# Optimization experiments

Measured on AMD Instinct MI355X. Metric: run time of the kernel, lower is better.

The kernel has to match this reference:

```python
import jax, jax.numpy as jnp
import numpy as np

EPS = 1e-7
B, C, H, W = 8, 128, 256, 256
HEADS, P = 8, 8
P2 = P * P  # 64
KSIZE = 3


def setup_inputs() -> dict:
    key = jax.random.key(0)
    ks = jax.random.split(key, 9)
    s = 0.05
    x = jax.random.normal(ks[0], (B, C, H, W), jnp.float32)
    Wq = jax.random.normal(ks[1], (P2 * HEADS, P2), jnp.float32) * s
    bq = jax.random.normal(ks[2], (P2 * HEADS,), jnp.float32) * s
    Wk = jax.random.normal(ks[3], (P2 * HEADS, P2), jnp.float32) * s
    bk = jax.random.normal(ks[4], (P2 * HEADS,), jnp.float32) * s
    Wv = jax.random.normal(ks[5], (C, C), jnp.float32) * s  # 1x1 conv squeezed
    bv = jax.random.normal(ks[6], (C,), jnp.float32) * s
    Wp = jax.random.normal(ks[7], (C, 1, KSIZE, KSIZE), jnp.float32) * s  # depthwise
    bp = jax.random.normal(ks[8], (C,), jnp.float32) * s
    return {"x": x, "Wq": Wq, "bq": bq, "Wk": Wk, "bk": bk,
            "Wv": Wv, "bv": bv, "Wp": Wp, "bp": bp}


def _linear_attn(q, k, xv):
    # q, k: [B, heads, C, P2]; xv: [B, heads, C, d2]
    l1, d1 = q.shape[-2], q.shape[-1]
    l2, d2 = xv.shape[-2], xv.shape[-1]
    if l1 * d1 * l2 + l1 * l2 * d2 <= d2 * l2 * d1 + d2 * d1 * l1:
        qk = jnp.einsum('bhcp,bhdp->bhcd', q, k)          # q @ k^T : [B,h,C,C]
        qk = qk / (qk.sum(axis=-1, keepdims=True) + EPS)
        return jnp.einsum('bhcd,bhde->bhce', qk, xv)
    else:
        kx = jnp.einsum('bhcp,bhcd->bhpd', k, xv)          # k^T @ x : [B,h,P2,d2]
        out = jnp.einsum('bhcp,bhpd->bhcd', q, kx)         # q @ (k^T @ x)
        denom = jnp.einsum('bhcp,bhp->bhc', q, k.sum(axis=2)) + EPS  # q @ rowsum(k^T)
        return out / denom[..., None]


def reference(x, Wq, bq, Wk, bk, Wv, bv, Wp, bp):
    Bs, Cs, Hs, Ws = x.shape
    # AdaptiveAvgPool2d(P) with divisible dims == block mean
    pooled = x.reshape(Bs, Cs, P, Hs // P, P, Ws // P).mean(axis=(3, 5))
    pooled = pooled.reshape(Bs, Cs, P2)
    q = jax.nn.relu(pooled @ Wq.T + bq).reshape(Bs, Cs, HEADS, P2).transpose(0, 2, 1, 3)
    k = jax.nn.relu(pooled @ Wk.T + bk).reshape(Bs, Cs, HEADS, P2).transpose(0, 2, 1, 3)
    # 1x1 conv (v)
    v = jnp.einsum('bchw,oc->bohw', x, Wv) + bv[None, :, None, None]
    d2 = (Hs * Ws) // HEADS  # divisible by construction -> no replicate pad
    xv = v.reshape(Bs, Cs, HEADS, d2).transpose(0, 2, 1, 3)
    attn = _linear_attn(q, k, xv)                           # [B,h,C,d2]
    out = attn.transpose(0, 2, 1, 3).reshape(Bs, Cs, Hs, Ws)
    # depthwise 3x3 proj, padding 1
    out = jax.lax.conv_general_dilated(
        out, Wp, window_strides=(1, 1), padding=[(1, 1), (1, 1)],
        dimension_numbers=('NCHW', 'OIHW', 'NCHW'), feature_group_count=Cs)
    return out + bp[None, :, None, None]
```

## Files before the change

### kernel.cpp

```cpp
#include <hip/hip_runtime.h>
#include <hip/hip_bf16.h>

#define HW 65536
#define CCH 128

typedef __attribute__((ext_vector_type(8))) short short8;
typedef __attribute__((ext_vector_type(4))) float f32x4;
typedef __attribute__((ext_vector_type(8))) unsigned short u16x8;

__device__ __forceinline__ void gload_lds16(const void* g, void* l) {
    __builtin_amdgcn_global_load_lds((const __attribute__((address_space(1))) void*)g,
                                     (__attribute__((address_space(3))) void*)l, 16, 0, 0);
}
__device__ __forceinline__ unsigned short f2bf(float f) {
    union { float f; unsigned int i; } u; u.f = f;
    unsigned int r = u.i + 0x7fffu + ((u.i >> 16) & 1u);
    return (unsigned short)(r >> 16);
}
__device__ __forceinline__ float bf2f(unsigned short h) {
    union { unsigned int i; float f; } u; u.i = ((unsigned int)h) << 16; return u.f;
}

__global__ __launch_bounds__(256) void pool_kernel(const float* __restrict__ x,
                                                   float* __restrict__ pooled) {
    int bc = blockIdx.x;
    const float* base = x + (size_t)bc * HW;
    int t = threadIdx.x;
    for (int py = 0; py < 8; ++py) {
        float acc = 0.f;
        const float* rowp = base + py * 32 * 256 + t;
        #pragma unroll
        for (int r = 0; r < 32; ++r) acc += rowp[r * 256];
        for (int off = 16; off > 0; off >>= 1) acc += __shfl_down(acc, off, 32);
        if ((t & 31) == 0)
            pooled[(size_t)bc * 64 + py * 8 + (t >> 5)] = acc * (1.0f / 1024.0f);
    }
}

__global__ __launch_bounds__(256) void qk_kernel(const float* __restrict__ pooled,
        const float* __restrict__ Wq, const float* __restrict__ bq,
        const float* __restrict__ Wk, const float* __restrict__ bk,
        float* __restrict__ qo, float* __restrict__ ko) {
    int bc = blockIdx.x;
    int t = threadIdx.x;
    __shared__ float ps[64];
    if (t < 64) ps[t] = pooled[(size_t)bc * 64 + t];
    __syncthreads();
    for (int m = 0; m < 2; ++m) {
        const float* W = m ? Wk : Wq;
        const float* bb = m ? bk : bq;
        float* o = m ? ko : qo;
        for (int oi = t; oi < 512; oi += 256) {
            float acc = bb[oi];
            const float* wr = W + oi * 64;
            #pragma unroll
            for (int p = 0; p < 64; ++p) acc += ps[p] * wr[p];
            o[(size_t)bc * 512 + oi] = fmaxf(acc, 0.f);
        }
    }
}

__global__ __launch_bounds__(256) void am1_kernel(const float* __restrict__ q,
        const float* __restrict__ k, const float* __restrict__ bv,
        unsigned short* __restrict__ Ahi, unsigned short* __restrict__ Alo,
        float* __restrict__ beta) {
    int bid = blockIdx.x;
    int bh = bid >> 2;
    int cg = bid & 3;
    int b = bh >> 3, h = bh & 7;
    int t = threadIdx.x;
    __shared__ float ks[128 * 68];
    __shared__ float qs[32 * 68];
    __shared__ float bvs[128];
    for (int i = t; i < 2048; i += 256) {
        int d = i >> 4, p4 = (i & 15) * 4;
        *(f32x4*)&ks[d * 68 + p4] = *(const f32x4*)(k + ((size_t)(b * CCH + d)) * 512 + h * 64 + p4);
    }
    for (int i = t; i < 512; i += 256) {
        int cl = i >> 4, p4 = (i & 15) * 4;
        *(f32x4*)&qs[cl * 68 + p4] = *(const f32x4*)(q + ((size_t)(b * CCH + cg * 32 + cl)) * 512 + h * 64 + p4);
    }
    if (t < 128) bvs[t] = bv[t];
    __syncthreads();
    int cl = t >> 3, dc = t & 7;
    int c = cg * 32 + cl;
    int d0 = dc * 16;
    f32x4 qr[16];
    #pragma unroll
    for (int ch = 0; ch < 16; ++ch) qr[ch] = *(const f32x4*)&qs[cl * 68 + ch * 4];
    float a[16];
    #pragma unroll
    for (int j = 0; j < 16; ++j) {
        int d = d0 + j;
        float acc = 0.f;
        #pragma unroll
        for (int ch = 0; ch < 16; ++ch) {
            f32x4 kr = *(const f32x4*)&ks[d * 68 + ch * 4];
            acc += qr[ch].x * kr.x + qr[ch].y * kr.y + qr[ch].z * kr.z + qr[ch].w * kr.w;
        }
        a[j] = acc;
    }
    float s = 0.f;
    #pragma unroll
    for (int j = 0; j < 16; ++j) s += a[j];
    s += __shfl_xor(s, 1);
    s += __shfl_xor(s, 2);
    s += __shfl_xor(s, 4);
    float inv = 1.0f / (s + 1e-7f);
    float bpart = 0.f;
    union { unsigned short u[16]; uint4 v[2]; } ph, pl;
    #pragma unroll
    for (int j = 0; j < 16; ++j) {
        float an = a[j] * inv;
        bpart += an * bvs[d0 + j];
        unsigned short hi = f2bf(an);
        ph.u[j] = hi;
        pl.u[j] = f2bf(an - bf2f(hi));
    }
    bpart += __shfl_xor(bpart, 1);
    bpart += __shfl_xor(bpart, 2);
    bpart += __shfl_xor(bpart, 4);
    if (dc == 0) beta[bh * 128 + c] = bpart;
    size_t ao = (size_t)bh * 16384 + c * 128 + d0;
    *(uint4*)(Ahi + ao) = ph.v[0];
    *(uint4*)(Ahi + ao + 8) = ph.v[1];
    *(uint4*)(Alo + ao) = pl.v[0];
    *(uint4*)(Alo + ao + 8) = pl.v[1];
}

__global__ __launch_bounds__(256) void wvt_kernel(const float* __restrict__ Wv,
        unsigned short* __restrict__ WvThi, unsigned short* __restrict__ WvTlo) {
    int idx = blockIdx.x * 256 + threadIdx.x;
    int d = idx >> 7, e = idx & 127;
    float v = Wv[d * 128 + e];
    unsigned short hi = f2bf(v);
    WvThi[e * 128 + d] = hi;
    WvTlo[e * 128 + d] = f2bf(v - bf2f(hi));
}

__global__ __launch_bounds__(256) void am2_kernel(
        const unsigned short* __restrict__ Ahi, const unsigned short* __restrict__ Alo,
        const unsigned short* __restrict__ WvThi, const unsigned short* __restrict__ WvTlo,
        unsigned short* __restrict__ Mo) {
    int bid = blockIdx.x;
    int bh = bid >> 1;
    int eg = bid & 1;
    int tid = threadIdx.x;
    int w = tid >> 6, l = tid & 63;
    int lc = l & 15, lk = (l >> 4) * 8;
    f32x4 acc[2][4] = {};
    const unsigned short* Ab = Ahi + (size_t)bh * 16384;
    const unsigned short* Alb = Alo + (size_t)bh * 16384;
    #pragma unroll
    for (int ksi = 0; ksi < 4; ++ksi) {
        int d = ksi * 32 + lk;
        short8 ah[2], al[2], bhv[4], blv[4];
        #pragma unroll
        for (int ci = 0; ci < 2; ++ci) {
            int c = w * 32 + ci * 16 + lc;
            ah[ci] = *(const short8*)(Ab + c * 128 + d);
            al[ci] = *(const short8*)(Alb + c * 128 + d);
        }
        #pragma unroll
        for (int ei = 0; ei < 4; ++ei) {
            int e = eg * 64 + ei * 16 + lc;
            bhv[ei] = *(const short8*)(WvThi + e * 128 + d);
            blv[ei] = *(const short8*)(WvTlo + e * 128 + d);
        }
        #pragma unroll
        for (int ci = 0; ci < 2; ++ci)
            #pragma unroll
            for (int ei = 0; ei < 4; ++ei) {
                acc[ci][ei] = __builtin_amdgcn_mfma_f32_16x16x32_bf16(ah[ci], bhv[ei], acc[ci][ei], 0, 0, 0);
                acc[ci][ei] = __builtin_amdgcn_mfma_f32_16x16x32_bf16(ah[ci], blv[ei], acc[ci][ei], 0, 0, 0);
                acc[ci][ei] = __builtin_amdgcn_mfma_f32_16x16x32_bf16(al[ci], bhv[ei], acc[ci][ei], 0, 0, 0);
            }
    }
    unsigned short* Mb = Mo + (size_t)bh * 16384;
    #pragma unroll
    for (int ci = 0; ci < 2; ++ci)
        #pragma unroll
        for (int ei = 0; ei < 4; ++ei)
            #pragma unroll
            for (int r = 0; r < 4; ++r) {
                int c = w * 32 + ci * 16 + (l >> 4) * 4 + r;
                int e = eg * 64 + ei * 16 + lc;
                Mb[c * 128 + e] = f2bf(acc[ci][ei][r]);
            }
}

__global__ __launch_bounds__(512, 4) void attn_kernel(
        const float* __restrict__ x,
        const __hip_bfloat16* __restrict__ Mbf,
        const float* __restrict__ beta,
        __hip_bfloat16* __restrict__ attn) {
    int bid = blockIdx.x;
    int bh = bid >> 4;
    int chunk = bid & 15;
    int b = bh >> 3, h = bh & 7;
    int s0g = h * 8192 + chunk * 512;
    int tid = threadIdx.x;
    int w = tid >> 6, l = tid & 63;

    __shared__ __align__(16) char sm[65536];
    char* ts0 = sm + 32768;

    const char* Mg = (const char*)(Mbf + (size_t)bh * 16384);
    #pragma unroll
    for (int i = 0; i < 4; ++i) {
        int o = i * 8192 + tid * 16;
        int osw = o ^ (((o >> 8) & 7) << 4);
        gload_lds16(Mg + osw, sm + o);
    }

    int e0u = (tid >> 4) * 2;
    int s4u = (tid & 15) * 4;
    const float* xb = x + (size_t)b * CCH * HW + s0g;

    f32x4 rg[4];
    #define LOADT(t_) do { \
        const float* p0 = xb + (size_t)e0u * HW + (t_) * 64 + s4u; \
        rg[0] = *(const f32x4*)p0; \
        rg[1] = *(const f32x4*)(p0 + HW); \
        const float* p1 = p0 + (size_t)64 * HW; \
        rg[2] = *(const f32x4*)p1; \
        rg[3] = *(const f32x4*)(p1 + HW); \
    } while (0)
    #define WRITET(buf_) do { \
        _Pragma("unroll") \
        for (int j = 0; j < 4; ++j) { \
            int s = s4u + j; \
            int sw = (s & 7) << 4; \
            unsigned int pa = (unsigned int)f2bf(rg[0][j]) | ((unsigned int)f2bf(rg[1][j]) << 16); \
            unsigned int pb = (unsigned int)f2bf(rg[2][j]) | ((unsigned int)f2bf(rg[3][j]) << 16); \
            *(unsigned int*)((buf_) + ((s * 256 + e0u * 2) ^ sw)) = pa; \
            *(unsigned int*)((buf_) + ((s * 256 + (e0u + 64) * 2) ^ sw)) = pb; \
        } \
    } while (0)

    LOADT(0);
    WRITET(ts0);
    LOADT(1);
    __syncthreads();

    int c0w = (w >> 1) * 32;
    int s0w = (w & 1) * 32;
    short8 mf[2][4];
    #pragma unroll
    for (int ci = 0; ci < 2; ++ci)
        #pragma unroll
        for (int ksi = 0; ksi < 4; ++ksi) {
            int c = c0w + ci * 16 + (l & 15);
            int o = (c * 256 + ksi * 64 + ((l >> 4) * 16)) ^ ((c & 7) << 4);
            mf[ci][ksi] = *(const short8*)(sm + o);
        }
    const float* bet = beta + bh * 128;
    float bv0 = bet[c0w + (l & 15)];
    float bv1 = bet[c0w + 16 + (l & 15)];
    __hip_bfloat16* ab = attn + (size_t)b * CCH * HW + s0g;

    for (int t = 0; t < 8; ++t) {
        char* tsc = ts0 + (t & 1) * 16384;
        if (t < 7) WRITET(ts0 + ((t + 1) & 1) * 16384);
        if (t < 6) LOADT(t + 2);
        f32x4 acc[2][2] = {};
        #pragma unroll
        for (int ksi = 0; ksi < 4; ++ksi) {
            short8 af[2];
            #pragma unroll
            for (int si = 0; si < 2; ++si) {
                int s = s0w + si * 16 + (l & 15);
                int o = (s * 256 + ksi * 64 + ((l >> 4) * 16)) ^ ((s & 7) << 4);
                af[si] = *(const short8*)(tsc + o);
            }
            #pragma unroll
            for (int si = 0; si < 2; ++si)
                #pragma unroll
                for (int ci = 0; ci < 2; ++ci)
                    acc[si][ci] = __builtin_amdgcn_mfma_f32_16x16x32_bf16(af[si], mf[ci][ksi], acc[si][ci], 0, 0, 0);
        }
        #pragma unroll
        for (int si = 0; si < 2; ++si)
            #pragma unroll
            for (int ci = 0; ci < 2; ++ci) {
                int sb = s0w + si * 16 + (l >> 4) * 4;
                int c = c0w + ci * 16 + (l & 15);
                float bvv = ci ? bv1 : bv0;
                union { unsigned short u[4]; uint2 v; } pk;
                #pragma unroll
                for (int r = 0; r < 4; ++r) pk.u[r] = f2bf(acc[si][ci][r] + bvv);
                *(uint2*)(ab + (size_t)c * HW + t * 64 + sb) = pk.v;
            }
        __syncthreads();
    }
    #undef LOADT
    #undef WRITET
}

__global__ __launch_bounds__(256) void dwconv_kernel(const __hip_bfloat16* __restrict__ attn,
        const float* __restrict__ Wp, const float* __restrict__ bp,
        float* __restrict__ out) {
    int bid = blockIdx.x;
    int bc = bid >> 3;
    int ys = bid & 7;
    int y0 = ys * 32;
    int t = threadIdx.x;
    __shared__ unsigned short tile[34][264];
    const unsigned short* base = (const unsigned short*)attn + (size_t)bc * HW;
    for (int i = t; i < 34 * 32; i += 256) {
        int r = i >> 5, ck = i & 31;
        int gy = y0 + r - 1;
        u16x8 v;
        if (gy >= 0 && gy < 256) v = *(const u16x8*)(base + gy * 256 + ck * 8);
        else v = (u16x8)((unsigned short)0);
        *(u16x8*)&tile[r][ck * 8] = v;
    }
    __syncthreads();
    int c = bc & 127;
    float wv[9];
    #pragma unroll
    for (int j = 0; j < 9; ++j) wv[j] = Wp[c * 9 + j];
    float bias = bp[c];
    float* obase = out + (size_t)bc * HW;
    for (int p = 0; p < 4; ++p) {
        int orow = p * 8 + (t >> 5);
        int oc = (t & 31) * 8;
        float accv[8];
        #pragma unroll
        for (int j = 0; j < 8; ++j) accv[j] = bias;
        #pragma unroll
        for (int dy = 0; dy < 3; ++dy) {
            int tr = orow + dy;
            u16x8 m = *(const u16x8*)&tile[tr][oc];
            float f[10];
            f[0] = (oc == 0) ? 0.f : bf2f(tile[tr][oc - 1]);
            #pragma unroll
            for (int j = 0; j < 8; ++j) f[j + 1] = bf2f(m[j]);
            f[9] = (oc == 248) ? 0.f : bf2f(tile[tr][oc + 8]);
            float w0 = wv[dy * 3], w1 = wv[dy * 3 + 1], w2 = wv[dy * 3 + 2];
            #pragma unroll
            for (int j = 0; j < 8; ++j)
                accv[j] += w0 * f[j] + w1 * f[j + 1] + w2 * f[j + 2];
        }
        float* op = obase + (size_t)(y0 + orow) * 256 + oc;
        float4 o0 = {accv[0], accv[1], accv[2], accv[3]};
        float4 o1 = {accv[4], accv[5], accv[6], accv[7]};
        *(float4*)op = o0;
        *(float4*)(op + 4) = o1;
    }
}

extern "C" void kernel_launch(void* const* d_in, const int* in_sizes, int n_in,
                              void* d_out, int out_size, void* d_ws, size_t ws_size,
                              hipStream_t stream) {
    const float* x  = (const float*)d_in[0];
    const float* Wq = (const float*)d_in[1];
    const float* bq = (const float*)d_in[2];
    const float* Wk = (const float*)d_in[3];
    const float* bk = (const float*)d_in[4];
    const float* Wv = (const float*)d_in[5];
    const float* bv = (const float*)d_in[6];
    const float* Wp = (const float*)d_in[7];
    const float* bp = (const float*)d_in[8];
    float* out = (float*)d_out;
    char* ws = (char*)d_ws;

    float* pooled = (float*)ws;
    float* qb     = (float*)(ws + 262144);
    float* kb     = (float*)(ws + 2359296);
    __hip_bfloat16* Mbf = (__hip_bfloat16*)(ws + 4456448);
    float* betab  = (float*)(ws + 6553600);
    char* attnp   = ws + 6586368;
    unsigned short* Ahi   = (unsigned short*)attnp;
    unsigned short* Alo   = (unsigned short*)(attnp + 2097152);
    unsigned short* WvThi = (unsigned short*)(attnp + 4194304);
    unsigned short* WvTlo = (unsigned short*)(attnp + 4227072);

    pool_kernel<<<dim3(1024), dim3(256), 0, stream>>>(x, pooled);
    qk_kernel<<<dim3(1024), dim3(256), 0, stream>>>(pooled, Wq, bq, Wk, bk, qb, kb);
    am1_kernel<<<dim3(256), dim3(256), 0, stream>>>(qb, kb, bv, Ahi, Alo, betab);
    wvt_kernel<<<dim3(64), dim3(256), 0, stream>>>(Wv, WvThi, WvTlo);
    am2_kernel<<<dim3(128), dim3(256), 0, stream>>>(Ahi, Alo, WvThi, WvTlo, (unsigned short*)Mbf);
    attn_kernel<<<dim3(1024), dim3(512), 0, stream>>>(x, Mbf, betab, (__hip_bfloat16*)attnp);
    dwconv_kernel<<<dim3(8192), dim3(256), 0, stream>>>((const __hip_bfloat16*)attnp, Wp, bp, out);
}
```

Measured before the change: 306.5 us.

## Fuse q/k projection into attention-matrix kernel, inline Wv transpose, vectorize pooling

Merges the q/k projection and the attention-matrix construction into one kernel, so q and k are computed straight into LDS and never written to or read back from global memory. The separate Wv transpose/split kernel is removed: each am2 block now builds a swizzled bf16 hi/lo copy of Wv in LDS itself. Pooling switches to f32x4 vector loads with a narrower shuffle reduction, and bf16 packing uses the hardware packed-convert instruction. Together these cut two kernel launches and some global traffic. In exchange, the k projection is recomputed per channel-group block (four times per batch-head), the fused kernel needs a large LDS footprint that may limit occupancy, and the packed convert's rounding may differ slightly from the manual round-to-nearest-even helper.

```diff
diff --git a/kernel.cpp b/kernel.cpp
--- a/kernel.cpp
+++ b/kernel.cpp
@@ -19,6 +19,11 @@
 }
 __device__ __forceinline__ float bf2f(unsigned short h) {
     union { unsigned int i; float f; } u; u.i = ((unsigned int)h) << 16; return u.f;
+}
+__device__ __forceinline__ unsigned int cvt_pk_bf16(float lo, float hi) {
+    unsigned int r;
+    asm("v_cvt_pk_bf16_f32 %0, %1, %2" : "=v"(r) : "v"(lo), "v"(hi));
+    return r;
 }
 
 __global__ __launch_bounds__(256) void pool_kernel(const float* __restrict__ x,
@@ -26,42 +31,32 @@
     int bc = blockIdx.x;
     const float* base = x + (size_t)bc * HW;
     int t = threadIdx.x;
-    for (int py = 0; py < 8; ++py) {
-        float acc = 0.f;
-        const float* rowp = base + py * 32 * 256 + t;
-        #pragma unroll
-        for (int r = 0; r < 32; ++r) acc += rowp[r * 256];
-        for (int off = 16; off > 0; off >>= 1) acc += __shfl_down(acc, off, 32);
-        if ((t & 31) == 0)
-            pooled[(size_t)bc * 64 + py * 8 + (t >> 5)] = acc * (1.0f / 1024.0f);
-    }
-}
-
-__global__ __launch_bounds__(256) void qk_kernel(const float* __restrict__ pooled,
+    int w = t >> 6, l = t & 63;
+    for (int it = 0; it < 2; ++it) {
+        int py = w + it * 4;
+        const float* rp = base + py * 32 * 256 + l * 4;
+        f32x4 s0 = {0.f, 0.f, 0.f, 0.f};
+        f32x4 s1 = {0.f, 0.f, 0.f, 0.f};
+        #pragma unroll
+        for (int r = 0; r < 32; r += 2) {
+            s0 += *(const f32x4*)(rp + r * 256);
+            s1 += *(const f32x4*)(rp + (r + 1) * 256);
+        }
+        f32x4 sv = s0 + s1;
+        float acc = sv[0] + sv[1] + sv[2] + sv[3];
+        acc += __shfl_down(acc, 4, 8);
+        acc += __shfl_down(acc, 2, 8);
+        acc += __shfl_down(acc, 1, 8);
+        if ((l & 7) == 0)
+            pooled[(size_t)bc * 64 + py * 8 + (l >> 3)] = acc * (1.0f / 1024.0f);
+    }
+}
+
+__global__ __launch_bounds__(256) void qkam_kernel(
+        const float* __restrict__ pooled,
         const float* __restrict__ Wq, const float* __restrict__ bq,
         const float* __restrict__ Wk, const float* __restrict__ bk,
-        float* __restrict__ qo, float* __restrict__ ko) {
-    int bc = blockIdx.x;
-    int t = threadIdx.x;
-    __shared__ float ps[64];
-    if (t < 64) ps[t] = pooled[(size_t)bc * 64 + t];
-    __syncthreads();
-    for (int m = 0; m < 2; ++m) {
-        const float* W = m ? Wk : Wq;
-        const float* bb = m ? bk : bq;
-        float* o = m ? ko : qo;
-        for (int oi = t; oi < 512; oi += 256) {
-            float acc = bb[oi];
-            const float* wr = W + oi * 64;
-            #pragma unroll
-            for (int p = 0; p < 64; ++p) acc += ps[p] * wr[p];
-            o[(size_t)bc * 512 + oi] = fmaxf(acc, 0.f);
-        }
-    }
-}
-
-__global__ __launch_bounds__(256) void am1_kernel(const float* __restrict__ q,
-        const float* __restrict__ k, const float* __restrict__ bv,
+        const float* __restrict__ bv,
         unsigned short* __restrict__ Ahi, unsigned short* __restrict__ Alo,
         float* __restrict__ beta) {
     int bid = blockIdx.x;
@@ -69,83 +64,129 @@
     int cg = bid & 3;
     int b = bh >> 3, h = bh & 7;
     int t = threadIdx.x;
+    __shared__ float ps[128 * 64];
+    __shared__ float Wqs[64 * 64];
+    __shared__ float Wks[64 * 64];
     __shared__ float ks[128 * 68];
     __shared__ float qs[32 * 68];
     __shared__ float bvs[128];
+
     for (int i = t; i < 2048; i += 256) {
-        int d = i >> 4, p4 = (i & 15) * 4;
-        *(f32x4*)&ks[d * 68 + p4] = *(const f32x4*)(k + ((size_t)(b * CCH + d)) * 512 + h * 64 + p4);
-    }
-    for (int i = t; i < 512; i += 256) {
-        int cl = i >> 4, p4 = (i & 15) * 4;
-        *(f32x4*)&qs[cl * 68 + p4] = *(const f32x4*)(q + ((size_t)(b * CCH + cg * 32 + cl)) * 512 + h * 64 + p4);
+        int c = i >> 4, p4 = (i & 15) * 4;
+        *(f32x4*)&ps[c * 64 + p4] = *(const f32x4*)(pooled + (size_t)(b * CCH + c) * 64 + p4);
+    }
+    for (int i = t; i < 1024; i += 256) {
+        int r = i >> 4, p4 = (i & 15) * 4;
+        *(f32x4*)&Wqs[r * 64 + p4] = *(const f32x4*)(Wq + (size_t)(h * 64 + r) * 64 + p4);
+        *(f32x4*)&Wks[r * 64 + p4] = *(const f32x4*)(Wk + (size_t)(h * 64 + r) * 64 + p4);
     }
     if (t < 128) bvs[t] = bv[t];
     __syncthreads();
-    int cl = t >> 3, dc = t & 7;
-    int c = cg * 32 + cl;
-    int d0 = dc * 16;
-    f32x4 qr[16];
-    #pragma unroll
-    for (int ch = 0; ch < 16; ++ch) qr[ch] = *(const f32x4*)&qs[cl * 68 + ch * 4];
-    float a[16];
-    #pragma unroll
-    for (int j = 0; j < 16; ++j) {
-        int d = d0 + j;
-        float acc = 0.f;
-        #pragma unroll
-        for (int ch = 0; ch < 16; ++ch) {
-            f32x4 kr = *(const f32x4*)&ks[d * 68 + ch * 4];
-            acc += qr[ch].x * kr.x + qr[ch].y * kr.y + qr[ch].z * kr.z + qr[ch].w * kr.w;
-        }
-        a[j] = acc;
-    }
-    float s = 0.f;
-    #pragma unroll
-    for (int j = 0; j < 16; ++j) s += a[j];
-    s += __shfl_xor(s, 1);
-    s += __shfl_xor(s, 2);
-    s += __shfl_xor(s, 4);
-    float inv = 1.0f / (s + 1e-7f);
-    float bpart = 0.f;
-    union { unsigned short u[16]; uint4 v[2]; } ph, pl;
-    #pragma unroll
-    for (int j = 0; j < 16; ++j) {
-        float an = a[j] * inv;
-        bpart += an * bvs[d0 + j];
-        unsigned short hi = f2bf(an);
-        ph.u[j] = hi;
-        pl.u[j] = f2bf(an - bf2f(hi));
-    }
-    bpart += __shfl_xor(bpart, 1);
-    bpart += __shfl_xor(bpart, 2);
-    bpart += __shfl_xor(bpart, 4);
-    if (dc == 0) beta[bh * 128 + c] = bpart;
-    size_t ao = (size_t)bh * 16384 + c * 128 + d0;
-    *(uint4*)(Ahi + ao) = ph.v[0];
-    *(uint4*)(Ahi + ao + 8) = ph.v[1];
-    *(uint4*)(Alo + ao) = pl.v[0];
-    *(uint4*)(Alo + ao + 8) = pl.v[1];
-}
-
-__global__ __launch_bounds__(256) void wvt_kernel(const float* __restrict__ Wv,
-        unsigned short* __restrict__ WvThi, unsigned short* __restrict__ WvTlo) {
-    int idx = blockIdx.x * 256 + threadIdx.x;
-    int d = idx >> 7, e = idx & 127;
-    float v = Wv[d * 128 + e];
-    unsigned short hi = f2bf(v);
-    WvThi[e * 128 + d] = hi;
-    WvTlo[e * 128 + d] = f2bf(v - bf2f(hi));
+
+    {
+        int p = t & 63, g = t >> 6;
+        f32x4 wr[16];
+        #pragma unroll
+        for (int j = 0; j < 16; ++j) wr[j] = *(const f32x4*)&Wks[p * 64 + j * 4];
+        float bkv = bk[h * 64 + p];
+        for (int dd = 0; dd < 32; ++dd) {
+            int d = g * 32 + dd;
+            float acc = bkv;
+            #pragma unroll
+            for (int j = 0; j < 16; ++j) {
+                f32x4 pv = *(const f32x4*)&ps[d * 64 + j * 4];
+                acc += pv[0] * wr[j][0] + pv[1] * wr[j][1] + pv[2] * wr[j][2] + pv[3] * wr[j][3];
+            }
+            ks[d * 68 + p] = fmaxf(acc, 0.f);
+        }
+        #pragma unroll
+        for (int j = 0; j < 16; ++j) wr[j] = *(const f32x4*)&Wqs[p * 64 + j * 4];
+        float bqv = bq[h * 64 + p];
+        for (int dd = 0; dd < 8; ++dd) {
+            int cl = g * 8 + dd;
+            int c = cg * 32 + cl;
+            float acc = bqv;
+            #pragma unroll
+            for (int j = 0; j < 16; ++j) {
+                f32x4 pv = *(const f32x4*)&ps[c * 64 + j * 4];
+                acc += pv[0] * wr[j][0] + pv[1] * wr[j][1] + pv[2] * wr[j][2] + pv[3] * wr[j][3];
+            }
+            qs[cl * 68 + p] = fmaxf(acc, 0.f);
+        }
+    }
+    __syncthreads();
+
+    {
+        int cl = t >> 3, dc = t & 7;
+        int c = cg * 32 + cl;
+        int d0 = dc * 16;
+        f32x4 qr[16];
+        #pragma unroll
+        for (int ch = 0; ch < 16; ++ch) qr[ch] = *(const f32x4*)&qs[cl * 68 + ch * 4];
+        float a[16];
+        #pragma unroll
+        for (int jr = 0; jr < 16; ++jr) {
+            int j = (jr + dc * 2) & 15;
+            int d = d0 + j;
+            float acc = 0.f;
+            #pragma unroll
+            for (int ch = 0; ch < 16; ++ch) {
+                f32x4 kr = *(const f32x4*)&ks[d * 68 + ch * 4];
+                acc += qr[ch][0] * kr[0] + qr[ch][1] * kr[1] + qr[ch][2] * kr[2] + qr[ch][3] * kr[3];
+            }
+            a[j] = acc;
+        }
+        float s = 0.f;
+        #pragma unroll
+        for (int j = 0; j < 16; ++j) s += a[j];
+        s += __shfl_xor(s, 1);
+        s += __shfl_xor(s, 2);
+        s += __shfl_xor(s, 4);
+        float inv = 1.0f / (s + 1e-7f);
+        float bpart = 0.f;
+        union { unsigned short u[16]; uint4 v[2]; } ph, pl;
+        #pragma unroll
+        for (int j = 0; j < 16; ++j) {
+            float an = a[j] * inv;
+            bpart += an * bvs[d0 + j];
+            unsigned short hi = f2bf(an);
+            ph.u[j] = hi;
+            pl.u[j] = f2bf(an - bf2f(hi));
+        }
+        bpart += __shfl_xor(bpart, 1);
+        bpart += __shfl_xor(bpart, 2);
+        bpart += __shfl_xor(bpart, 4);
+        if (dc == 0) beta[bh * 128 + c] = bpart;
+        size_t ao = (size_t)bh * 16384 + c * 128 + d0;
+        *(uint4*)(Ahi + ao) = ph.v[0];
+        *(uint4*)(Ahi + ao + 8) = ph.v[1];
+        *(uint4*)(Alo + ao) = pl.v[0];
+        *(uint4*)(Alo + ao + 8) = pl.v[1];
+    }
 }
 
 __global__ __launch_bounds__(256) void am2_kernel(
         const unsigned short* __restrict__ Ahi, const unsigned short* __restrict__ Alo,
-        const unsigned short* __restrict__ WvThi, const unsigned short* __restrict__ WvTlo,
-        unsigned short* __restrict__ Mo) {
+        const float* __restrict__ Wv, unsigned short* __restrict__ Mo) {
     int bid = blockIdx.x;
     int bh = bid >> 1;
     int eg = bid & 1;
     int tid = threadIdx.x;
+    __shared__ __align__(16) char Wt[65536];
+    for (int i = tid; i < 4096; i += 256) {
+        int d = i >> 5, e4 = (i & 31) * 4;
+        f32x4 v = *(const f32x4*)(Wv + (size_t)d * 128 + e4);
+        #pragma unroll
+        for (int j = 0; j < 4; ++j) {
+            int e = e4 + j;
+            unsigned short hi = f2bf(v[j]);
+            unsigned short lo = f2bf(v[j] - bf2f(hi));
+            int o = (e * 256 + d * 2) ^ ((e & 7) << 4);
+            *(unsigned short*)(Wt + o) = hi;
+            *(unsigned short*)(Wt + 32768 + o) = lo;
+        }
+    }
+    __syncthreads();
     int w = tid >> 6, l = tid & 63;
     int lc = l & 15, lk = (l >> 4) * 8;
     f32x4 acc[2][4] = {};
@@ -164,8 +205,9 @@
         #pragma unroll
         for (int ei = 0; ei < 4; ++ei) {
             int e = eg * 64 + ei * 16 + lc;
-            bhv[ei] = *(const short8*)(WvThi + e * 128 + d);
-            blv[ei] = *(const short8*)(WvTlo + e * 128 + d);
+            int o = (e * 256 + d * 2) ^ ((e & 7) << 4);
+            bhv[ei] = *(const short8*)(Wt + o);
+            blv[ei] = *(const short8*)(Wt + 32768 + o);
         }
         #pragma unroll
         for (int ci = 0; ci < 2; ++ci)
@@ -231,8 +273,8 @@
         for (int j = 0; j < 4; ++j) { \
             int s = s4u + j; \
             int sw = (s & 7) << 4; \
-            unsigned int pa = (unsigned int)f2bf(rg[0][j]) | ((unsigned int)f2bf(rg[1][j]) << 16); \
-            unsigned int pb = (unsigned int)f2bf(rg[2][j]) | ((unsigned int)f2bf(rg[3][j]) << 16); \
+            unsigned int pa = cvt_pk_bf16(rg[0][j], rg[1][j]); \
+            unsigned int pb = cvt_pk_bf16(rg[2][j], rg[3][j]); \
             *(unsigned int*)((buf_) + ((s * 256 + e0u * 2) ^ sw)) = pa; \
             *(unsigned int*)((buf_) + ((s * 256 + (e0u + 64) * 2) ^ sw)) = pb; \
         } \
@@ -286,10 +328,10 @@
                 int sb = s0w + si * 16 + (l >> 4) * 4;
                 int c = c0w + ci * 16 + (l & 15);
                 float bvv = ci ? bv1 : bv0;
-                union { unsigned short u[4]; uint2 v; } pk;
-                #pragma unroll
-                for (int r = 0; r < 4; ++r) pk.u[r] = f2bf(acc[si][ci][r] + bvv);
-                *(uint2*)(ab + (size_t)c * HW + t * 64 + sb) = pk.v;
+                uint2 pk2;
+                pk2.x = cvt_pk_bf16(acc[si][ci][0] + bvv, acc[si][ci][1] + bvv);
+                pk2.y = cvt_pk_bf16(acc[si][ci][2] + bvv, acc[si][ci][3] + bvv);
+                *(uint2*)(ab + (size_t)c * HW + t * 64 + sb) = pk2;
             }
         __syncthreads();
     }
@@ -365,22 +407,16 @@
     float* out = (float*)d_out;
     char* ws = (char*)d_ws;
 
-    float* pooled = (float*)ws;
-    float* qb     = (float*)(ws + 262144);
-    float* kb     = (float*)(ws + 2359296);
-    __hip_bfloat16* Mbf = (__hip_bfloat16*)(ws + 4456448);
-    float* betab  = (float*)(ws + 6553600);
-    char* attnp   = ws + 6586368;
-    unsigned short* Ahi   = (unsigned short*)attnp;
-    unsigned short* Alo   = (unsigned short*)(attnp + 2097152);
-    unsigned short* WvThi = (unsigned short*)(attnp + 4194304);
-    unsigned short* WvTlo = (unsigned short*)(attnp + 4227072);
+    float* pooled      = (float*)ws;
+    unsigned short* Ahi = (unsigned short*)(ws + 262144);
+    unsigned short* Alo = (unsigned short*)(ws + 2359296);
+    unsigned short* Mo  = (unsigned short*)(ws + 4456448);
+    float* betab       = (float*)(ws + 6553600);
+    char* attnp        = ws + 6586368;
 
     pool_kernel<<<dim3(1024), dim3(256), 0, stream>>>(x, pooled);
-    qk_kernel<<<dim3(1024), dim3(256), 0, stream>>>(pooled, Wq, bq, Wk, bk, qb, kb);
-    am1_kernel<<<dim3(256), dim3(256), 0, stream>>>(qb, kb, bv, Ahi, Alo, betab);
-    wvt_kernel<<<dim3(64), dim3(256), 0, stream>>>(Wv, WvThi, WvTlo);
-    am2_kernel<<<dim3(128), dim3(256), 0, stream>>>(Ahi, Alo, WvThi, WvTlo, (unsigned short*)Mbf);
-    attn_kernel<<<dim3(1024), dim3(512), 0, stream>>>(x, Mbf, betab, (__hip_bfloat16*)attnp);
+    qkam_kernel<<<dim3(256), dim3(256), 0, stream>>>(pooled, Wq, bq, Wk, bk, bv, Ahi, Alo, betab);
+    am2_kernel<<<dim3(128), dim3(256), 0, stream>>>(Ahi, Alo, Wv, Mo);
+    attn_kernel<<<dim3(1024), dim3(512), 0, stream>>>(x, (const __hip_bfloat16*)Mo, betab, (__hip_bfloat16*)attnp);
     dwconv_kernel<<<dim3(8192), dim3(256), 0, stream>>>((const __hip_bfloat16*)attnp, Wp, bp, out);
 }
```

Result: faster. 274.2 us (-10.5%).
